# Kernel optimization log

Measured on AMD Instinct MI355X. Metric: run time of the kernel, lower is better.

## Reference

```python
import jax, jax.numpy as jnp
import numpy as np
import math

EXP_HALF = math.exp(-0.5)  # constant scale exp(-1/2) from the original module


def setup_inputs() -> dict:
    key = jax.random.key(0)
    k1, k2, k3, k4 = jax.random.split(key, 4)
    T, N, DR2 = 32, 4096, 512
    all_data_static = jax.random.normal(k1, (T, N, DR2), dtype=jnp.float32)
    threshold_nc = jax.random.uniform(k2, (T, N, 1), dtype=jnp.float32)
    all_data_dynamic_now = jax.random.uniform(k3, (N, DR2), dtype=jnp.float32)
    # w1 initialized RandomNormal(mean=1.0, stddev=0.5) as in build()
    w1 = 1.0 + 0.5 * jax.random.normal(k4, (2 * DR2, DR2), dtype=jnp.float32)
    smooth_gate_logit = jnp.full((1,), -0.5, dtype=jnp.float32)
    smooth_scale = jnp.full((1,), 0.5, dtype=jnp.float32)
    return {
        "all_data_static": all_data_static,
        "threshold_nc": threshold_nc,
        "all_data_dynamic_now": all_data_dynamic_now,
        "w1": w1,
        "smooth_gate_logit": smooth_gate_logit,
        "smooth_scale": smooth_scale,
    }


def _evolve(all_data_static, threshold_nc, h0, w1, smooth_gate_logit, smooth_scale):
    def step(h, inputs):
        s_i, thr_i = inputs  # s_i: [N, DR2], thr_i: [N, 1]
        z = jnp.concatenate([h, s_i], axis=-1) @ w1  # [N, DR2]
        cand = jax.nn.sigmoid(z * thr_i + h * (1.0 - thr_i)) * EXP_HALF
        delta = jnp.mean(jnp.abs(cand - h), axis=-1, keepdims=True)  # [N, 1]
        g = jax.nn.sigmoid(smooth_gate_logit + smooth_scale * delta)
        h_new = g * h + (1.0 - g) * cand
        return h_new, h_new

    _, states = jax.lax.scan(step, h0, (all_data_static, threshold_nc))
    # states: [T, N, DR2] -- state after each of the T gated updates
    all_data_dynamic = states
    h_final = states[-1]
    all_data_dynamic_diff = states[1:] - states[:-1]  # [T-1, N, DR2]
    return all_data_dynamic, h_final, all_data_dynamic_diff


def reference(all_data_static, threshold_nc, all_data_dynamic_now, w1,
              smooth_gate_logit, smooth_scale):
    return _evolve(all_data_static, threshold_nc, all_data_dynamic_now, w1,
                   smooth_gate_logit, smooth_scale)
```

## Files before the change

kernel.cpp:

```cpp
#include <hip/hip_runtime.h>

typedef __attribute__((ext_vector_type(4))) float f32x4;

#define T_STEPS 32
#define NROWS 4096
#define DR2 512
#define EXP_HALF 0.6065306597126334f

#define OUT_HFINAL 67108864ul
#define OUT_DIFF   69206016ul
#define SLOT_F32   2097152ul

__device__ __forceinline__ unsigned char f2fp8(float f) {
  return (unsigned char)__builtin_amdgcn_cvt_pk_fp8_f32(f, f, 0, false);
}

__device__ __forceinline__ void barrier_lds() {
  asm volatile("s_waitcnt lgkmcnt(0)" ::: "memory");
  __builtin_amdgcn_s_barrier();
  asm volatile("" ::: "memory");
}

__device__ __forceinline__ float* zs_slot(float* out, int t) {
  return out + (t < 31 ? OUT_DIFF + (size_t)t * SLOT_F32 : OUT_HFINAL);
}
__device__ __forceinline__ unsigned char* zs_blk8(float* out, int t, int eb) {
  return (unsigned char*)zs_slot(out, t) + (size_t)eb * 32768;
}


__global__ __launch_bounds__(256) void quant_w1(const float* __restrict__ w1,
                                                unsigned char* __restrict__ w1f) {
  const int half = blockIdx.x >> 5;
  const int ct   = blockIdx.x & 31;
  const int l15  = threadIdx.x & 15;
  const int kk   = threadIdx.x >> 4;
  const int col  = ct * 16 + l15;
  const int K0   = half * 512;
#pragma unroll
  for (int lg = 0; lg < 4; lg++) {
    unsigned long long v = 0;
#pragma unroll
    for (int e = 0; e < 8; e++) {
      int k = K0 + kk * 32 + lg * 8 + e;
      unsigned long long b = f2fp8(w1[(size_t)k * 512 + col]);
      v |= b << (8 * e);
    }
    *(unsigned long long*)(w1f + (size_t)half * 262144 + ct * 8192 + kk * 512
                           + lg * 128 + l15 * 8) = v;
  }
}

__global__ __launch_bounds__(1024) void dense_zs(
    const float* __restrict__ s_all,
    const unsigned char* __restrict__ w1f,
    float* __restrict__ out)
{
  __shared__ __align__(16) unsigned char A_lds[2][8192];
  const int tid  = threadIdx.x;
  const int lane = tid & 63;
  const int wave = tid >> 6;
  const int l15  = lane & 15;
  const int lg   = lane >> 4;
  const int t    = blockIdx.x >> 5;
  const int rc   = blockIdx.x & 31;

  long Bv[2][16];
#pragma unroll
  for (int n = 0; n < 2; n++)
#pragma unroll
    for (int kk = 0; kk < 16; kk++)
      Bv[n][kk] = *(const long*)(w1f + 262144
                   + (size_t)(wave * 2 + n) * 8192 + kk * 512 + lane * 8);

  const int di = (lane >> 2) * 512 + (lane & 3) * 128
               + ((wave ^ l15) & 15) * 8;
  const float* srow = s_all + ((size_t)t * NROWS + rc * 128 + wave) * DR2 + lane * 8;

  float4 v0 = *(const float4*)srow;
  float4 v1 = *(const float4*)(srow + 4);
  {
    int pa = __builtin_amdgcn_cvt_pk_fp8_f32(v0.x, v0.y, 0, false);
    int pw0 = __builtin_amdgcn_cvt_pk_fp8_f32(v0.z, v0.w, pa, true);
    int pb = __builtin_amdgcn_cvt_pk_fp8_f32(v1.x, v1.y, 0, false);
    int pw1 = __builtin_amdgcn_cvt_pk_fp8_f32(v1.z, v1.w, pb, true);
    *(uint2*)(A_lds[0] + di) = make_uint2((unsigned)pw0, (unsigned)pw1);
  }
  barrier_lds();

#pragma unroll
  for (int j = 0; j < 8; j++) {
    if (j < 7) {
      const float* p = srow + (size_t)(j + 1) * 16 * DR2;
      v0 = *(const float4*)p;
      v1 = *(const float4*)(p + 4);
    }
    f32x4 acc[2];
#pragma unroll
    for (int n = 0; n < 2; n++)
#pragma unroll
      for (int i = 0; i < 4; i++) acc[n][i] = -256.0f;
    const unsigned char* buf = A_lds[j & 1];
#pragma unroll
    for (int kk = 0; kk < 16; kk++) {
      long a = *(const long*)(buf + kk * 512 + lg * 128
                              + ((l15 ^ ((kk * 4 + lg) & 15)) << 3));
      acc[0] = __builtin_amdgcn_mfma_f32_16x16x32_fp8_fp8(a, Bv[0][kk], acc[0], 0, 0, 0);
      acc[1] = __builtin_amdgcn_mfma_f32_16x16x32_fp8_fp8(a, Bv[1][kk], acc[1], 0, 0, 0);
    }
    int p0 = __builtin_amdgcn_cvt_pk_fp8_f32(acc[0][0], acc[0][1], 0, false);
    p0 = __builtin_amdgcn_cvt_pk_fp8_f32(acc[0][2], acc[0][3], p0, true);
    int p1 = __builtin_amdgcn_cvt_pk_fp8_f32(acc[1][0], acc[1][1], 0, false);
    p1 = __builtin_amdgcn_cvt_pk_fp8_f32(acc[1][2], acc[1][3], p1, true);
    *(uint2*)(zs_blk8(out, t, rc * 8 + j) + (size_t)tid * 8) =
        make_uint2((unsigned)p0, (unsigned)p1);

    if (j < 7) {
      int pa = __builtin_amdgcn_cvt_pk_fp8_f32(v0.x, v0.y, 0, false);
      int pw0 = __builtin_amdgcn_cvt_pk_fp8_f32(v0.z, v0.w, pa, true);
      int pb = __builtin_amdgcn_cvt_pk_fp8_f32(v1.x, v1.y, 0, false);
      int pw1 = __builtin_amdgcn_cvt_pk_fp8_f32(v1.z, v1.w, pb, true);
      *(uint2*)(A_lds[(j + 1) & 1] + di) = make_uint2((unsigned)pw0, (unsigned)pw1);
      barrier_lds();
    }
  }
}

__global__ __attribute__((amdgpu_flat_work_group_size(1024, 1024),
                          amdgpu_waves_per_eu(4, 4)))
void evolve_fp8(
    const float* __restrict__ thr_all,
    const float* __restrict__ h0,
    const unsigned char* __restrict__ w1f,
    const float* __restrict__ p_logit,
    const float* __restrict__ p_scale,
    float* __restrict__ out)
{
  constexpr int R = 16;
  __shared__ __align__(16) unsigned char A_lds[8192];
  __shared__ float thr_lds[T_STEPS * R];
  __shared__ float partial[R][17];

  const int tid  = threadIdx.x;
  const int lane = tid & 63;
  const int wave = tid >> 6;
  const int l15  = lane & 15;
  const int lg   = lane >> 4;
  const int brow0 = blockIdx.x * R;
  const int colbase = wave * 32 + l15;

  const float glogit = *p_logit;
  const float gscale = *p_scale;

  long Bv[2][16];
#pragma unroll
  for (int n = 0; n < 2; n++)
#pragma unroll
    for (int kk = 0; kk < 16; kk++)
      Bv[n][kk] = *(const long*)(w1f + (size_t)(wave * 2 + n) * 8192
                                 + kk * 512 + lane * 8);

  f32x4 h[2];
#pragma unroll
  for (int n = 0; n < 2; n++)
#pragma unroll
    for (int i = 0; i < 4; i++)
      h[n][i] = h0[(size_t)(brow0 + lg * 4 + i) * DR2 + colbase + n * 16];

  if (tid < T_STEPS * R)
    thr_lds[tid] = thr_all[(size_t)(tid >> 4) * NROWS + brow0 + (tid & 15)];

  uint2 zraw = *(const uint2*)(zs_blk8(out, 0, blockIdx.x) + (size_t)tid * 8);

#pragma unroll 1
  for (int t = 0; t < T_STEPS; t++) {
#pragma unroll
    for (int n = 0; n < 2; n++) {
      int c = colbase + n * 16;
      int base = (c >> 5) * 512 + ((c >> 3) & 3) * 128 + (c & 7);
      int x = (c >> 3) & 15;
#pragma unroll
      for (int i = 0; i < 4; i++) {
        int r = lg * 4 + i;
        A_lds[base + ((r ^ x) & 15) * 8] = f2fp8(h[n][i]);
      }
    }
    uint2 znext;
    if (t + 1 < T_STEPS)
      znext = *(const uint2*)(zs_blk8(out, t + 1, blockIdx.x) + (size_t)tid * 8);
    barrier_lds();

    f32x4 acc[2];
#pragma unroll
    for (int n = 0; n < 2; n++)
#pragma unroll
      for (int i = 0; i < 4; i++) acc[n][i] = 256.0f;
#pragma unroll
    for (int kk = 0; kk < 16; kk++) {
      long a = *(const long*)(A_lds + kk * 512 + lg * 128
                              + ((l15 ^ ((kk * 4 + lg) & 15)) << 3));
      acc[0] = __builtin_amdgcn_mfma_f32_16x16x32_fp8_fp8(a, Bv[0][kk], acc[0], 0, 0, 0);
      acc[1] = __builtin_amdgcn_mfma_f32_16x16x32_fp8_fp8(a, Bv[1][kk], acc[1], 0, 0, 0);
    }
    {
      const unsigned int zw[2] = { zraw.x, zraw.y };
#pragma unroll
      for (int j = 0; j < 8; j++) {
        unsigned int b = (zw[j >> 2] >> ((j & 3) * 8)) & 0xffu;
        unsigned int man = (b & 0x7fu) << 20;
        unsigned int bits = ((b & 0x80u) << 24) | (man + (120u << 23));
        acc[j >> 2][j & 3] += __uint_as_float(bits);
      }
    }

    f32x4 cand[2];
#pragma unroll
    for (int i = 0; i < 4; i++) {
      int r = lg * 4 + i;
      float th = thr_lds[t * R + r];
      float s = 0.f;
#pragma unroll
      for (int n = 0; n < 2; n++) {
        float hh = h[n][i];
        float x  = acc[n][i] * th + hh * (1.0f - th);
        float c  = EXP_HALF / (1.0f + __expf(-x));
        cand[n][i] = c;
        s += fabsf(c - hh);
      }
      s += __shfl_xor(s, 1);
      s += __shfl_xor(s, 2);
      s += __shfl_xor(s, 4);
      s += __shfl_xor(s, 8);
      if (l15 == 0) partial[r][wave] = s;
    }
    barrier_lds();

    float tot = partial[l15][lg] + partial[l15][lg + 4]
              + partial[l15][lg + 8] + partial[l15][lg + 12];
    tot += __shfl_xor(tot, 16);
    tot += __shfl_xor(tot, 32);
    float gme = 1.0f / (1.0f + __expf(-(glogit + gscale * (tot * (1.0f / 512.0f)))));

    const size_t srowbase = (size_t)t * NROWS + brow0;
#pragma unroll
    for (int i = 0; i < 4; i++) {
      int r = lg * 4 + i;
      float g = __shfl(gme, r);
#pragma unroll
      for (int n = 0; n < 2; n++) {
        int c = colbase + n * 16;
        float hh = h[n][i];
        float hn = g * hh + (1.0f - g) * cand[n][i];
        h[n][i] = hn;
        out[(srowbase + r) * DR2 + c] = hn;
        if (t > 0) out[OUT_DIFF + (srowbase - NROWS + r) * DR2 + c] = hn - hh;
      }
    }
    if (t == T_STEPS - 1) {
#pragma unroll
      for (int i = 0; i < 4; i++) {
        int r = lg * 4 + i;
#pragma unroll
        for (int n = 0; n < 2; n++)
          out[OUT_HFINAL + (size_t)(brow0 + r) * DR2 + colbase + n * 16] = h[n][i];
      }
    }
    zraw = znext;
  }
}

extern "C" void kernel_launch(void* const* d_in, const int* in_sizes, int n_in,
                              void* d_out, int out_size, void* d_ws, size_t ws_size,
                              hipStream_t stream) {
  const float* s_all   = (const float*)d_in[0];
  const float* thr_all = (const float*)d_in[1];
  const float* h0      = (const float*)d_in[2];
  const float* w1      = (const float*)d_in[3];
  const float* p_logit = (const float*)d_in[4];
  const float* p_scale = (const float*)d_in[5];
  float* out = (float*)d_out;

  unsigned char* w1f = (unsigned char*)d_ws;

  hipLaunchKernelGGL(quant_w1, dim3(64), dim3(256), 0, stream, w1, w1f);
  hipLaunchKernelGGL(dense_zs, dim3(1024), dim3(1024), 0, stream, s_all, w1f, out);
  hipLaunchKernelGGL(evolve_fp8, dim3(256), dim3(1024), 0, stream,
                     thr_all, h0, w1f, p_logit, p_scale, out);
}
```

Baseline: 294.8 us.

## Fuse static-input GEMM into evolve kernel, keeping half of zs in LDS

Removes the separate dense_zs kernel. Each evolve block now first computes its own 16 rows of s@W1_bottom for all 32 time steps, keeping the first 16 steps of fp8 results in LDS (128KB) and spilling the rest to global scratch. The recurrent loop then reads zs from LDS or global. This drops one launch and part of the global round trip. In exchange, only 256 blocks do the static GEMM instead of 1024, and the larger LDS footprint may limit occupancy.

```diff
diff --git a/kernel.cpp b/kernel.cpp
--- a/kernel.cpp
+++ b/kernel.cpp
@@ -3,6 +3,7 @@
 typedef __attribute__((ext_vector_type(4))) float f32x4;
 
 #define T_STEPS 32
+#define T_LDS   16
 #define NROWS 4096
 #define DR2 512
 #define EXP_HALF 0.6065306597126334f
@@ -51,84 +52,10 @@
   }
 }
 
-__global__ __launch_bounds__(1024) void dense_zs(
-    const float* __restrict__ s_all,
-    const unsigned char* __restrict__ w1f,
-    float* __restrict__ out)
-{
-  __shared__ __align__(16) unsigned char A_lds[2][8192];
-  const int tid  = threadIdx.x;
-  const int lane = tid & 63;
-  const int wave = tid >> 6;
-  const int l15  = lane & 15;
-  const int lg   = lane >> 4;
-  const int t    = blockIdx.x >> 5;
-  const int rc   = blockIdx.x & 31;
-
-  long Bv[2][16];
-#pragma unroll
-  for (int n = 0; n < 2; n++)
-#pragma unroll
-    for (int kk = 0; kk < 16; kk++)
-      Bv[n][kk] = *(const long*)(w1f + 262144
-                   + (size_t)(wave * 2 + n) * 8192 + kk * 512 + lane * 8);
-
-  const int di = (lane >> 2) * 512 + (lane & 3) * 128
-               + ((wave ^ l15) & 15) * 8;
-  const float* srow = s_all + ((size_t)t * NROWS + rc * 128 + wave) * DR2 + lane * 8;
-
-  float4 v0 = *(const float4*)srow;
-  float4 v1 = *(const float4*)(srow + 4);
-  {
-    int pa = __builtin_amdgcn_cvt_pk_fp8_f32(v0.x, v0.y, 0, false);
-    int pw0 = __builtin_amdgcn_cvt_pk_fp8_f32(v0.z, v0.w, pa, true);
-    int pb = __builtin_amdgcn_cvt_pk_fp8_f32(v1.x, v1.y, 0, false);
-    int pw1 = __builtin_amdgcn_cvt_pk_fp8_f32(v1.z, v1.w, pb, true);
-    *(uint2*)(A_lds[0] + di) = make_uint2((unsigned)pw0, (unsigned)pw1);
-  }
-  barrier_lds();
-
-#pragma unroll
-  for (int j = 0; j < 8; j++) {
-    if (j < 7) {
-      const float* p = srow + (size_t)(j + 1) * 16 * DR2;
-      v0 = *(const float4*)p;
-      v1 = *(const float4*)(p + 4);
-    }
-    f32x4 acc[2];
-#pragma unroll
-    for (int n = 0; n < 2; n++)
-#pragma unroll
-      for (int i = 0; i < 4; i++) acc[n][i] = -256.0f;
-    const unsigned char* buf = A_lds[j & 1];
-#pragma unroll
-    for (int kk = 0; kk < 16; kk++) {
-      long a = *(const long*)(buf + kk * 512 + lg * 128
-                              + ((l15 ^ ((kk * 4 + lg) & 15)) << 3));
-      acc[0] = __builtin_amdgcn_mfma_f32_16x16x32_fp8_fp8(a, Bv[0][kk], acc[0], 0, 0, 0);
-      acc[1] = __builtin_amdgcn_mfma_f32_16x16x32_fp8_fp8(a, Bv[1][kk], acc[1], 0, 0, 0);
-    }
-    int p0 = __builtin_amdgcn_cvt_pk_fp8_f32(acc[0][0], acc[0][1], 0, false);
-    p0 = __builtin_amdgcn_cvt_pk_fp8_f32(acc[0][2], acc[0][3], p0, true);
-    int p1 = __builtin_amdgcn_cvt_pk_fp8_f32(acc[1][0], acc[1][1], 0, false);
-    p1 = __builtin_amdgcn_cvt_pk_fp8_f32(acc[1][2], acc[1][3], p1, true);
-    *(uint2*)(zs_blk8(out, t, rc * 8 + j) + (size_t)tid * 8) =
-        make_uint2((unsigned)p0, (unsigned)p1);
-
-    if (j < 7) {
-      int pa = __builtin_amdgcn_cvt_pk_fp8_f32(v0.x, v0.y, 0, false);
-      int pw0 = __builtin_amdgcn_cvt_pk_fp8_f32(v0.z, v0.w, pa, true);
-      int pb = __builtin_amdgcn_cvt_pk_fp8_f32(v1.x, v1.y, 0, false);
-      int pw1 = __builtin_amdgcn_cvt_pk_fp8_f32(v1.z, v1.w, pb, true);
-      *(uint2*)(A_lds[(j + 1) & 1] + di) = make_uint2((unsigned)pw0, (unsigned)pw1);
-      barrier_lds();
-    }
-  }
-}
-
 __global__ __attribute__((amdgpu_flat_work_group_size(1024, 1024),
                           amdgpu_waves_per_eu(4, 4)))
-void evolve_fp8(
+void evolve_fused(
+    const float* __restrict__ s_all,
     const float* __restrict__ thr_all,
     const float* __restrict__ h0,
     const unsigned char* __restrict__ w1f,
@@ -136,23 +63,86 @@
     const float* __restrict__ p_scale,
     float* __restrict__ out)
 {
-  constexpr int R = 16;
-  __shared__ __align__(16) unsigned char A_lds[8192];
-  __shared__ float thr_lds[T_STEPS * R];
-  __shared__ float partial[R][17];
+  __shared__ __align__(16) unsigned char zs_lds[T_LDS * 8192];
+  __shared__ __align__(16) unsigned char A_lds[2][8192];
+  __shared__ float thr_lds[T_STEPS * 16];
+  __shared__ float partial[16][17];
 
   const int tid  = threadIdx.x;
   const int lane = tid & 63;
   const int wave = tid >> 6;
   const int l15  = lane & 15;
   const int lg   = lane >> 4;
-  const int brow0 = blockIdx.x * R;
+  const int brow0 = blockIdx.x * 16;
   const int colbase = wave * 32 + l15;
 
-  const float glogit = *p_logit;
-  const float gscale = *p_scale;
+  if (tid < T_STEPS * 16)
+    thr_lds[tid] = thr_all[(size_t)(tid >> 4) * NROWS + brow0 + (tid & 15)];
 
   long Bv[2][16];
+#pragma unroll
+  for (int n = 0; n < 2; n++)
+#pragma unroll
+    for (int kk = 0; kk < 16; kk++)
+      Bv[n][kk] = *(const long*)(w1f + 262144
+                   + (size_t)(wave * 2 + n) * 8192 + kk * 512 + lane * 8);
+
+  const int di = (lane >> 2) * 512 + (lane & 3) * 128
+               + ((wave ^ l15) & 15) * 8;
+  const float* sbase = s_all + ((size_t)brow0 + wave) * DR2 + lane * 8;
+
+  float4 v0 = *(const float4*)sbase;
+  float4 v1 = *(const float4*)(sbase + 4);
+  {
+    int pa = __builtin_amdgcn_cvt_pk_fp8_f32(v0.x, v0.y, 0, false);
+    int pw0 = __builtin_amdgcn_cvt_pk_fp8_f32(v0.z, v0.w, pa, true);
+    int pb = __builtin_amdgcn_cvt_pk_fp8_f32(v1.x, v1.y, 0, false);
+    int pw1 = __builtin_amdgcn_cvt_pk_fp8_f32(v1.z, v1.w, pb, true);
+    *(uint2*)(A_lds[0] + di) = make_uint2((unsigned)pw0, (unsigned)pw1);
+  }
+  barrier_lds();
+
+#pragma unroll 2
+  for (int t = 0; t < T_STEPS; t++) {
+    if (t < T_STEPS - 1) {
+      const float* p = sbase + (size_t)(t + 1) * NROWS * DR2;
+      v0 = *(const float4*)p;
+      v1 = *(const float4*)(p + 4);
+    }
+    f32x4 acc[2];
+#pragma unroll
+    for (int n = 0; n < 2; n++)
+#pragma unroll
+      for (int i = 0; i < 4; i++) acc[n][i] = -256.0f;
+    const unsigned char* buf = A_lds[t & 1];
+#pragma unroll
+    for (int kk = 0; kk < 16; kk++) {
+      long a = *(const long*)(buf + kk * 512 + lg * 128
+                              + ((l15 ^ ((kk * 4 + lg) & 15)) << 3));
+      acc[0] = __builtin_amdgcn_mfma_f32_16x16x32_fp8_fp8(a, Bv[0][kk], acc[0], 0, 0, 0);
+      acc[1] = __builtin_amdgcn_mfma_f32_16x16x32_fp8_fp8(a, Bv[1][kk], acc[1], 0, 0, 0);
+    }
+    int p0 = __builtin_amdgcn_cvt_pk_fp8_f32(acc[0][0], acc[0][1], 0, false);
+    p0 = __builtin_amdgcn_cvt_pk_fp8_f32(acc[0][2], acc[0][3], p0, true);
+    int p1 = __builtin_amdgcn_cvt_pk_fp8_f32(acc[1][0], acc[1][1], 0, false);
+    p1 = __builtin_amdgcn_cvt_pk_fp8_f32(acc[1][2], acc[1][3], p1, true);
+
+    if (t < T_STEPS - 1) {
+      int pa = __builtin_amdgcn_cvt_pk_fp8_f32(v0.x, v0.y, 0, false);
+      int pw0 = __builtin_amdgcn_cvt_pk_fp8_f32(v0.z, v0.w, pa, true);
+      int pb = __builtin_amdgcn_cvt_pk_fp8_f32(v1.x, v1.y, 0, false);
+      int pw1 = __builtin_amdgcn_cvt_pk_fp8_f32(v1.z, v1.w, pb, true);
+      *(uint2*)(A_lds[(t + 1) & 1] + di) = make_uint2((unsigned)pw0, (unsigned)pw1);
+    }
+    if (t < T_LDS)
+      *(uint2*)(zs_lds + t * 8192 + (size_t)tid * 8) =
+          make_uint2((unsigned)p0, (unsigned)p1);
+    else
+      *(uint2*)(zs_blk8(out, t, blockIdx.x) + (size_t)tid * 8) =
+          make_uint2((unsigned)p0, (unsigned)p1);
+    barrier_lds();
+  }
+
 #pragma unroll
   for (int n = 0; n < 2; n++)
 #pragma unroll
@@ -167,10 +157,10 @@
     for (int i = 0; i < 4; i++)
       h[n][i] = h0[(size_t)(brow0 + lg * 4 + i) * DR2 + colbase + n * 16];
 
-  if (tid < T_STEPS * R)
-    thr_lds[tid] = thr_all[(size_t)(tid >> 4) * NROWS + brow0 + (tid & 15)];
-
-  uint2 zraw = *(const uint2*)(zs_blk8(out, 0, blockIdx.x) + (size_t)tid * 8);
+  const float glogit = *p_logit;
+  const float gscale = *p_scale;
+
+  uint2 zraw = make_uint2(0u, 0u), znext = make_uint2(0u, 0u);
 
 #pragma unroll 1
   for (int t = 0; t < T_STEPS; t++) {
@@ -182,11 +172,10 @@
 #pragma unroll
       for (int i = 0; i < 4; i++) {
         int r = lg * 4 + i;
-        A_lds[base + ((r ^ x) & 15) * 8] = f2fp8(h[n][i]);
-      }
-    }
-    uint2 znext;
-    if (t + 1 < T_STEPS)
+        A_lds[0][base + ((r ^ x) & 15) * 8] = f2fp8(h[n][i]);
+      }
+    }
+    if (t + 1 >= T_LDS && t + 1 < T_STEPS)
       znext = *(const uint2*)(zs_blk8(out, t + 1, blockIdx.x) + (size_t)tid * 8);
     barrier_lds();
 
@@ -197,13 +186,18 @@
       for (int i = 0; i < 4; i++) acc[n][i] = 256.0f;
 #pragma unroll
     for (int kk = 0; kk < 16; kk++) {
-      long a = *(const long*)(A_lds + kk * 512 + lg * 128
+      long a = *(const long*)(A_lds[0] + kk * 512 + lg * 128
                               + ((l15 ^ ((kk * 4 + lg) & 15)) << 3));
       acc[0] = __builtin_amdgcn_mfma_f32_16x16x32_fp8_fp8(a, Bv[0][kk], acc[0], 0, 0, 0);
       acc[1] = __builtin_amdgcn_mfma_f32_16x16x32_fp8_fp8(a, Bv[1][kk], acc[1], 0, 0, 0);
     }
+    uint2 zr;
+    if (t < T_LDS)
+      zr = *(const uint2*)(zs_lds + t * 8192 + (size_t)tid * 8);
+    else
+      zr = zraw;
     {
-      const unsigned int zw[2] = { zraw.x, zraw.y };
+      const unsigned int zw[2] = { zr.x, zr.y };
 #pragma unroll
       for (int j = 0; j < 8; j++) {
         unsigned int b = (zw[j >> 2] >> ((j & 3) * 8)) & 0xffu;
@@ -217,7 +211,7 @@
 #pragma unroll
     for (int i = 0; i < 4; i++) {
       int r = lg * 4 + i;
-      float th = thr_lds[t * R + r];
+      float th = thr_lds[t * 16 + r];
       float s = 0.f;
 #pragma unroll
       for (int n = 0; n < 2; n++) {
@@ -283,7 +277,6 @@
   unsigned char* w1f = (unsigned char*)d_ws;
 
   hipLaunchKernelGGL(quant_w1, dim3(64), dim3(256), 0, stream, w1, w1f);
-  hipLaunchKernelGGL(dense_zs, dim3(1024), dim3(1024), 0, stream, s_all, w1f, out);
-  hipLaunchKernelGGL(evolve_fp8, dim3(256), dim3(1024), 0, stream,
-                     thr_all, h0, w1f, p_logit, p_scale, out);
-}
+  hipLaunchKernelGGL(evolve_fused, dim3(256), dim3(1024), 0, stream,
+                     s_all, thr_all, h0, w1f, p_logit, p_scale, out);
+}
```

Result: faster. 258.1 us, median of 4 (-12.4%).
